# Kernel optimization log

Hardware: AMD Instinct MI355X
Metric: run time of the kernel (lower is better)

Reference implementation:

```python
import jax, jax.numpy as jnp
import numpy as np

B = 2; QD = 128; H = QD; W = QD; NQ = QD * QD
EMBED = 256; HEADS = 8; POINTS = 4; D = EMBED // HEADS; FFN = 512


def setup_inputs() -> dict:
    key = jax.random.key(0)
    ks = jax.random.split(key, 16)
    s = 0.02
    rn = lambda k, shp: jax.random.normal(k, shp, jnp.float32) * s
    return {
        'q': jax.random.normal(ks[0], (B, NQ, EMBED), jnp.float32),
        'W_off': rn(ks[1], (EMBED, HEADS * POINTS * 2)),
        'b_off': rn(ks[2], (HEADS * POINTS * 2,)),
        'W_attn': rn(ks[3], (EMBED, HEADS * POINTS)),
        'b_attn': rn(ks[4], (HEADS * POINTS,)),
        'W_val': rn(ks[5], (EMBED, EMBED)),
        'b_val': rn(ks[6], (EMBED,)),
        'W_out': rn(ks[7], (EMBED, EMBED)),
        'b_out': rn(ks[8], (EMBED,)),
        'W1': rn(ks[9], (EMBED, FFN)),
        'b1': rn(ks[10], (FFN,)),
        'W2': rn(ks[11], (FFN, EMBED)),
        'b2': rn(ks[12], (EMBED,)),
        'gamma': jnp.ones((EMBED,), jnp.float32),
        'beta': jnp.zeros((EMBED,), jnp.float32),
    }


def _layernorm(x, g, b):
    m = x.mean(-1, keepdims=True)
    v = ((x - m) ** 2).mean(-1, keepdims=True)
    return (x - m) * jax.lax.rsqrt(v + 1e-5) * g + b


def _msda(q, W_off, b_off, W_attn, b_attn, W_val, b_val, W_out, b_out):
    # value projection; value == query here. (B, NQ, EMBED)
    value = q @ W_val + b_val
    v = value.reshape(B, NQ, HEADS, D).transpose(0, 2, 1, 3)  # (B, heads, Nv, D)

    off = (q @ W_off + b_off).reshape(B, NQ, HEADS, POINTS, 2)
    aw = jax.nn.softmax((q @ W_attn + b_attn).reshape(B, NQ, HEADS, POINTS), axis=-1)

    # reference points: torch.meshgrid(linspace, linspace, indexing='xy')
    lin = jnp.linspace(0.0, 1.0, QD)
    gx, gy = jnp.meshgrid(lin, lin, indexing='xy')
    ref = jnp.stack([gx, gy], -1).reshape(1, NQ, 1, 1, 2)

    # offset_normalizer = [W, H]; sampling locations in [0,1]
    loc = ref + off / jnp.array([W, H], jnp.float32)
    # grid_sample bilinear, align_corners=False: pixel = loc * size - 0.5
    px = (loc[..., 0] * W - 0.5).transpose(0, 2, 1, 3)  # (B, heads, NQ, P)
    py = (loc[..., 1] * H - 0.5).transpose(0, 2, 1, 3)

    x0 = jnp.floor(px)
    y0 = jnp.floor(py)
    sampled = jnp.zeros((B, HEADS, NQ, POINTS, D), jnp.float32)
    for dy in (0.0, 1.0):
        for dx in (0.0, 1.0):
            xi = x0 + dx
            yi = y0 + dy
            wgt = (1.0 - jnp.abs(px - xi)) * (1.0 - jnp.abs(py - yi))
            valid = ((xi >= 0) & (xi <= W - 1) & (yi >= 0) & (yi <= H - 1)).astype(jnp.float32)
            idx = (jnp.clip(yi, 0, H - 1).astype(jnp.int32) * W
                   + jnp.clip(xi, 0, W - 1).astype(jnp.int32))  # (B, heads, NQ, P)
            g = jnp.take_along_axis(v, idx.reshape(B, HEADS, NQ * POINTS, 1), axis=2)
            g = g.reshape(B, HEADS, NQ, POINTS, D)
            sampled = sampled + g * (wgt * valid)[..., None]

    awt = aw.transpose(0, 2, 1, 3)  # (B, heads, NQ, P)
    out = (sampled * awt[..., None]).sum(3)  # (B, heads, NQ, D)
    out = out.transpose(0, 2, 1, 3).reshape(B, NQ, EMBED)
    # mmcv: dropout(output_proj(out)) + identity ; dropout is identity at eval
    return out @ W_out + b_out + q


def reference(q, W_off, b_off, W_attn, b_attn, W_val, b_val, W_out, b_out,
              W1, b1, W2, b2, gamma, beta):
    attn = _msda(q, W_off, b_off, W_attn, b_attn, W_val, b_val, W_out, b_out)
    x = attn + q  # outer residual in the module (in addition to mmcv's internal one)
    ffn = _layernorm(jax.nn.relu(x @ W1 + b1) @ W2 + b2, gamma, beta)
    return x + ffn
```

## Files before the change

### kernel.cpp

```cpp
#include <hip/hip_runtime.h>
#include <hip/hip_bf16.h>
#include <cstddef>
#include <cstdint>

#define B_      2
#define QD_     128
#define NQ_     (QD_ * QD_)
#define EMBED_  256
#define HEADS_  8
#define POINTS_ 4
#define FFN_    512
#define RTOT_   (B_ * NQ_)
#define NCATP_  384

using bf16x8 = __attribute__((ext_vector_type(8))) short;
using f32x4  = __attribute__((ext_vector_type(4))) float;

__device__ __forceinline__ short f2bf(float f) {
    unsigned u = __float_as_uint(f);
    u += 0x7FFFu + ((u >> 16) & 1u);
    return (short)(u >> 16);
}
__device__ __forceinline__ float bf2f(short s) {
    return __uint_as_float(((unsigned)(unsigned short)s) << 16);
}

#define GLDS(gp, lp) __builtin_amdgcn_global_load_lds( \
        (const __attribute__((address_space(1))) void*)(gp), \
        (__attribute__((address_space(3))) void*)(lp), 16, 0, 0)

#define WCAT_ELEMS  (NCATP_ * 256)
#define WOUT_ELEMS  (256 * 256)
#define W1_ELEMS    (512 * 256)
#define W2_ELEMS    (256 * 512)
#define PREP_TOTAL  (WCAT_ELEMS + WOUT_ELEMS + W1_ELEMS + W2_ELEMS)
#define PREP_BLOCKS ((PREP_TOTAL + 255) / 256)

__global__ __launch_bounds__(256) void prep_weights(
        const float* __restrict__ Wv, const float* __restrict__ Wo,
        const float* __restrict__ Wa, const float* __restrict__ bv,
        const float* __restrict__ bo, const float* __restrict__ ba,
        const float* __restrict__ W_out, const float* __restrict__ W1,
        const float* __restrict__ W2,
        short* __restrict__ WcatT, short* __restrict__ WoutT,
        short* __restrict__ W1T, short* __restrict__ W2T,
        float* __restrict__ bcat) {
    int idx = blockIdx.x * 256 + threadIdx.x;
    if (idx < WCAT_ELEMS) {
        int c = idx >> 8, k = idx & 255;
        float v = 0.f;
        if (c < 256)      v = Wv[k * 256 + c];
        else if (c < 320) v = Wo[k * 64 + (c - 256)];
        else if (c < 352) v = Wa[k * 32 + (c - 320)];
        WcatT[idx] = f2bf(v);
    } else if (idx < WCAT_ELEMS + WOUT_ELEMS) {
        int j = idx - WCAT_ELEMS; int c = j >> 8, k = j & 255;
        WoutT[j] = f2bf(W_out[k * 256 + c]);
    } else if (idx < WCAT_ELEMS + WOUT_ELEMS + W1_ELEMS) {
        int j = idx - (WCAT_ELEMS + WOUT_ELEMS); int c = j >> 8, k = j & 255;
        W1T[j] = f2bf(W1[k * 512 + c]);
    } else if (idx < PREP_TOTAL) {
        int j = idx - (WCAT_ELEMS + WOUT_ELEMS + W1_ELEMS); int c = j >> 9, k = j & 511;
        W2T[j] = f2bf(W2[k * 256 + c]);
    }
    if (idx < NCATP_) {
        float v = 0.f;
        if (idx < 256)      v = bv[idx];
        else if (idx < 320) v = bo[idx - 256];
        else if (idx < 352) v = ba[idx - 320];
        bcat[idx] = v;
    }
}

__global__ __launch_bounds__(512) void gemm1_fused(
        const float* __restrict__ q,
        const short* __restrict__ WcatT,
        const float* __restrict__ bcat,
        short* __restrict__ qbf,
        short* __restrict__ vcomp,
        float* __restrict__ pm) {
    __shared__ __align__(16) short xs[128 * 256];
    __shared__ __align__(16) short Bs[2][128 * 64];

    const int t    = threadIdx.x;
    const int ln   = t & 63;
    const int w    = t >> 6;
    const int wr   = w >> 2;
    const int wc   = w & 3;
    const int lrow = ln & 15;
    const int lkg  = ln >> 4;
    const int row0 = blockIdx.x * 128;
    const int orow = lkg * 4;
    const int ocol = lrow;

    auto stage_b = [&](int step, int buf) {
        const int p  = step >> 2;
        const int kt = step & 3;
        #pragma unroll
        for (int j = 0; j < 2; ++j) {
            const int c0 = (w * 2 + j) * 64;
            const int c  = c0 + ln;
            const int r  = c >> 3;
            const int s  = (c & 7) ^ (r & 7);
            GLDS(WcatT + (size_t)(p * 128 + r) * 256 + kt * 64 + s * 8,
                 &Bs[buf][c0 * 8]);
        }
    };

    stage_b(0, 0);
    #pragma unroll
    for (int j = 0; j < 8; ++j) {
        const int c = t + 512 * j;
        const int r = c >> 5;
        const int s = c & 31;
        const float* qp = q + (size_t)(row0 + r) * 256 + s * 8;
        const float4 f0 = *(const float4*)qp;
        const float4 f1 = *(const float4*)(qp + 4);
        bf16x8 v;
        v[0] = f2bf(f0.x); v[1] = f2bf(f0.y); v[2] = f2bf(f0.z); v[3] = f2bf(f0.w);
        v[4] = f2bf(f1.x); v[5] = f2bf(f1.y); v[6] = f2bf(f1.z); v[7] = f2bf(f1.w);
        *(bf16x8*)&qbf[(size_t)(row0 + r) * 256 + s * 8] = v;
        const int kt = s >> 3, sc = s & 7;
        *(bf16x8*)&xs[kt * 8192 + r * 64 + (sc ^ (r & 7)) * 8] = v;
    }
    __syncthreads();

    f32x4 acc[4][2] = {};
    const f32x4 zero = {0.f, 0.f, 0.f, 0.f};

    int buf = 0;
    #pragma unroll 1
    for (int step = 0; step < 12; ++step) {
        if (step < 11) stage_b(step + 1, buf ^ 1);
        const int kt = step & 3;
        #pragma unroll
        for (int ks = 0; ks < 2; ++ks) {
            const int slot = ((ks * 4 + lkg) ^ (lrow & 7)) * 8;
            bf16x8 af[4], bfr[2];
            #pragma unroll
            for (int m = 0; m < 4; ++m)
                af[m] = *(const bf16x8*)&xs[kt * 8192 + (wr * 64 + m * 16 + lrow) * 64 + slot];
            #pragma unroll
            for (int n = 0; n < 2; ++n)
                bfr[n] = *(const bf16x8*)&Bs[buf][(wc * 32 + n * 16 + lrow) * 64 + slot];
            #pragma unroll
            for (int m = 0; m < 4; ++m)
                #pragma unroll
                for (int n = 0; n < 2; ++n)
                    acc[m][n] = __builtin_amdgcn_mfma_f32_16x16x32_bf16(
                        af[m], bfr[n], acc[m][n], 0, 0, 0);
        }
        __syncthreads();
        if ((step & 3) == 3) {
            const int p = step >> 2;
            #pragma unroll
            for (int m = 0; m < 4; ++m) {
                #pragma unroll
                for (int n = 0; n < 2; ++n) {
                    const int gcol = p * 128 + wc * 32 + n * 16 + ocol;
                    const float bv = bcat[gcol];
                    #pragma unroll
                    for (int rr = 0; rr < 4; ++rr) {
                        const int row = wr * 64 + m * 16 + orow + rr;
                        const float v = acc[m][n][rr] + bv;
                        if (gcol < 256) {
                            vcomp[(size_t)(row0 + row) * 256 + gcol] = f2bf(v);
                        } else {
                            const int cc = gcol - 256;
                            if (cc < 96)
                                pm[(size_t)(row0 + row) * 128 + cc] = v;
                        }
                    }
                    acc[m][n] = zero;
                }
            }
        }
        buf ^= 1;
    }
}

__global__ __launch_bounds__(512) void gemm_x_ffn1(
        const short* __restrict__ msda,
        const short* __restrict__ WoutT,
        const float* __restrict__ b_out,
        const short* __restrict__ qbf,
        const short* __restrict__ W1T,
        const float* __restrict__ b1,
        short* __restrict__ xbf,
        short* __restrict__ hid) {
    __shared__ __align__(16) short xs[128 * 256];
    __shared__ __align__(16) short stg[128 * 192];
    short* As = stg;
    short* Bs = stg + 128 * 64;

    const int t    = threadIdx.x;
    const int ln   = t & 63;
    const int w    = t >> 6;
    const int wr   = w >> 2;
    const int wc   = w & 3;
    const int lrow = ln & 15;
    const int lkg  = ln >> 4;
    const int row0 = blockIdx.x * 128;
    const int orow = lkg * 4;
    const int ocol = lrow;

    f32x4 acc[4][4] = {};
    for (int kt = 0; kt < 4; ++kt) {
        #pragma unroll
        for (int j = 0; j < 2; ++j) {
            const int c0 = (w * 2 + j) * 64;
            const int cc = c0 + ln;
            const int r  = cc >> 3;
            const int s  = (cc & 7) ^ (r & 7);
            GLDS(msda + (size_t)(row0 + r) * 256 + kt * 64 + s * 8, &As[c0 * 8]);
        }
        #pragma unroll
        for (int j = 0; j < 4; ++j) {
            const int c0 = (w * 4 + j) * 64;
            const int cc = c0 + ln;
            const int r  = cc >> 3;
            const int s  = (cc & 7) ^ (r & 7);
            GLDS(WoutT + (size_t)r * 256 + kt * 64 + s * 8, &Bs[c0 * 8]);
        }
        __syncthreads();
        #pragma unroll
        for (int ks = 0; ks < 2; ++ks) {
            const int slot = ((ks * 4 + lkg) ^ (lrow & 7)) * 8;
            bf16x8 af[4], bfr[4];
            #pragma unroll
            for (int m = 0; m < 4; ++m)
                af[m] = *(const bf16x8*)&As[(wr * 64 + m * 16 + lrow) * 64 + slot];
            #pragma unroll
            for (int n = 0; n < 4; ++n)
                bfr[n] = *(const bf16x8*)&Bs[(wc * 64 + n * 16 + lrow) * 64 + slot];
            #pragma unroll
            for (int m = 0; m < 4; ++m)
                #pragma unroll
                for (int n = 0; n < 4; ++n)
                    acc[m][n] = __builtin_amdgcn_mfma_f32_16x16x32_bf16(
                        af[m], bfr[n], acc[m][n], 0, 0, 0);
        }
        __syncthreads();
    }

    #pragma unroll
    for (int m = 0; m < 4; ++m) {
        #pragma unroll
        for (int n = 0; n < 4; ++n) {
            const int kk  = n * 16 + ocol;
            const int col = wc * 64 + kk;
            const float bv = b_out[col];
            #pragma unroll
            for (int rr = 0; rr < 4; ++rr) {
                const int row = wr * 64 + m * 16 + orow + rr;
                float v = acc[m][n][rr] + bv
                        + 2.f * bf2f(qbf[(size_t)(row0 + row) * 256 + col]);
                const short bb = f2bf(v);
                xbf[(size_t)(row0 + row) * 256 + col] = bb;
                xs[wc * 8192 + row * 64 + ((kk >> 3) ^ (row & 7)) * 8 + (kk & 7)] = bb;
            }
        }
    }
    __syncthreads();

    #pragma unroll 1
    for (int p = 0; p < 2; ++p) {
        f32x4 acc2[4][4] = {};
        for (int kt = 0; kt < 4; ++kt) {
            #pragma unroll
            for (int j = 0; j < 4; ++j) {
                const int c0 = (w * 4 + j) * 64;
                const int cc = c0 + ln;
                const int r  = cc >> 3;
                const int s  = (cc & 7) ^ (r & 7);
                GLDS(W1T + (size_t)(p * 256 + r) * 256 + kt * 64 + s * 8, &Bs[c0 * 8]);
            }
            __syncthreads();
            #pragma unroll
            for (int ks = 0; ks < 2; ++ks) {
                const int slot = ((ks * 4 + lkg) ^ (lrow & 7)) * 8;
                bf16x8 af[4], bfr[4];
                #pragma unroll
                for (int m = 0; m < 4; ++m)
                    af[m] = *(const bf16x8*)&xs[kt * 8192 + (wr * 64 + m * 16 + lrow) * 64 + slot];
                #pragma unroll
                for (int n = 0; n < 4; ++n)
                    bfr[n] = *(const bf16x8*)&Bs[(wc * 64 + n * 16 + lrow) * 64 + slot];
                #pragma unroll
                for (int m = 0; m < 4; ++m)
                    #pragma unroll
                    for (int n = 0; n < 4; ++n)
                        acc2[m][n] = __builtin_amdgcn_mfma_f32_16x16x32_bf16(
                            af[m], bfr[n], acc2[m][n], 0, 0, 0);
            }
            __syncthreads();
        }
        #pragma unroll
        for (int m = 0; m < 4; ++m) {
            #pragma unroll
            for (int n = 0; n < 4; ++n) {
                const int col = p * 256 + wc * 64 + n * 16 + ocol;
                const float bv = b1[col];
                #pragma unroll
                for (int rr = 0; rr < 4; ++rr) {
                    const int row = wr * 64 + m * 16 + orow + rr;
                    hid[(size_t)(row0 + row) * 512 + col] =
                        f2bf(fmaxf(acc2[m][n][rr] + bv, 0.f));
                }
            }
        }
    }
}

__global__ __launch_bounds__(256) void gemm_ln(
        const short* __restrict__ A,
        const short* __restrict__ Bt,
        const float* __restrict__ bias,
        const short* __restrict__ xres,
        const float* __restrict__ gamma, const float* __restrict__ beta,
        float* __restrict__ out, int M, int K) {
    __shared__ __align__(16) short As[2][64 * 64];
    __shared__ __align__(16) short Bs[256 * 64];
    __shared__ float red[64][4][2];

    const int t    = threadIdx.x;
    const int ln   = t & 63;
    const int w    = t >> 6;
    const int lrow = ln & 15;
    const int lkg  = ln >> 4;
    const int row0 = blockIdx.x * 64;

    f32x4 acc[4][4] = {};

    auto stage_a = [&](int buf, int k0) {
        #pragma unroll
        for (int j = 0; j < 2; ++j) {
            const int c0 = (w * 2 + j) * 64;
            const int c  = c0 + ln;
            const int r  = c >> 3;
            const int s  = (c & 7) ^ (r & 7);
            GLDS(A + (size_t)(row0 + r) * K + (k0 + s * 8), &As[buf][c0 * 8]);
        }
    };
    auto stage_b = [&](int k0) {
        #pragma unroll
        for (int j = 0; j < 8; ++j) {
            const int c0 = (w * 8 + j) * 64;
            const int c  = c0 + ln;
            const int r  = c >> 3;
            const int s  = (c & 7) ^ (r & 7);
            GLDS(Bt + (size_t)r * K + (k0 + s * 8), &Bs[c0 * 8]);
        }
    };

    stage_a(0, 0);
    stage_b(0);
    __syncthreads();
    int buf = 0;
    for (int kt = 0; kt < 8; ++kt) {
        if (kt < 7) stage_a(buf ^ 1, kt * 64 + 64);
        #pragma unroll
        for (int ks = 0; ks < 2; ++ks) {
            const int slot = ((ks * 4 + lkg) ^ (lrow & 7)) * 8;
            bf16x8 af[4], bfr[4];
            #pragma unroll
            for (int m = 0; m < 4; ++m)
                af[m] = *(const bf16x8*)&As[buf][(m * 16 + lrow) * 64 + slot];
            #pragma unroll
            for (int n = 0; n < 4; ++n)
                bfr[n] = *(const bf16x8*)&Bs[(w * 64 + n * 16 + lrow) * 64 + slot];
            #pragma unroll
            for (int m = 0; m < 4; ++m)
                #pragma unroll
                for (int n = 0; n < 4; ++n)
                    acc[m][n] = __builtin_amdgcn_mfma_f32_16x16x32_bf16(
                        af[m], bfr[n], acc[m][n], 0, 0, 0);
        }
        __syncthreads();
        if (kt < 7) {
            stage_b(kt * 64 + 64);
            __syncthreads();
        }
        buf ^= 1;
    }

    const int orow = lkg * 4;
    const int ocol = lrow;

    #pragma unroll
    for (int n = 0; n < 4; ++n) {
        const float bv = bias[w * 64 + n * 16 + ocol];
        #pragma unroll
        for (int m = 0; m < 4; ++m)
            #pragma unroll
            for (int rr = 0; rr < 4; ++rr)
                acc[m][n][rr] += bv;
    }

    #pragma unroll
    for (int m = 0; m < 4; ++m) {
        #pragma unroll
        for (int rr = 0; rr < 4; ++rr) {
            float s = 0.f, sq = 0.f;
            #pragma unroll
            for (int n = 0; n < 4; ++n) {
                const float v = acc[m][n][rr];
                s += v; sq += v * v;
            }
            #pragma unroll
            for (int o = 1; o < 16; o <<= 1) {
                s  += __shfl_xor(s, o, 64);
                sq += __shfl_xor(sq, o, 64);
            }
            if (ocol == 0) {
                const int row = m * 16 + orow + rr;
                red[row][w][0] = s;
                red[row][w][1] = sq;
            }
        }
    }
    __syncthreads();

    #pragma unroll
    for (int m = 0; m < 4; ++m) {
        #pragma unroll
        for (int rr = 0; rr < 4; ++rr) {
            const int row = m * 16 + orow + rr;
            const float S  = red[row][0][0] + red[row][1][0] + red[row][2][0] + red[row][3][0];
            const float SQ = red[row][0][1] + red[row][1][1] + red[row][2][1] + red[row][3][1];
            const float mean = S * (1.0f / 256.0f);
            const float var  = SQ * (1.0f / 256.0f) - mean * mean;
            const float rs   = rsqrtf(var + 1e-5f);
            const size_t rbase = (size_t)(row0 + row) * 256;
            #pragma unroll
            for (int n = 0; n < 4; ++n) {
                const int col = w * 64 + n * 16 + ocol;
                out[rbase + col] = bf2f(xres[rbase + col])
                                 + (acc[m][n][rr] - mean) * rs * gamma[col] + beta[col];
            }
        }
    }
}

__global__ __launch_bounds__(256) void msda_sample(
        const float* __restrict__ pm, const short* __restrict__ vcomp,
        short* __restrict__ msda) {
    __shared__ int   s_off[8][32][4];
    __shared__ float s_c[8][32][4];

    const int t  = threadIdx.x;
    const int r0 = blockIdx.x * 8;
    const int bq = r0 >> 14;

    {
        const int g = t >> 5, cmb = t & 31, h = cmb >> 2, p = cmb & 3;
        const int r = r0 + g;
        const int n = r & (NQ_ - 1);
        const int gi = n >> 7, gj = n & 127;
        const float* pr = pm + (size_t)r * 128;

        const float l0 = pr[64 + h * 4 + 0], l1 = pr[64 + h * 4 + 1];
        const float l2 = pr[64 + h * 4 + 2], l3 = pr[64 + h * 4 + 3];
        const float mx = fmaxf(fmaxf(l0, l1), fmaxf(l2, l3));
        const float sum = expf(l0 - mx) + expf(l1 - mx) + expf(l2 - mx) + expf(l3 - mx);
        const float lp = pr[64 + h * 4 + p];
        const float aw = expf(lp - mx) / sum;

        const float ox = pr[h * 8 + p * 2 + 0];
        const float oy = pr[h * 8 + p * 2 + 1];
        const float px = (gj * (1.0f / 127.0f) + ox * (1.0f / 128.0f)) * 128.0f - 0.5f;
        const float py = (gi * (1.0f / 127.0f) + oy * (1.0f / 128.0f)) * 128.0f - 0.5f;
        const float x0f = floorf(px), y0f = floorf(py);
        const int   x0 = (int)x0f, y0 = (int)y0f;
        const float fx = px - x0f, fy = py - y0f;
        const int x0c = min(max(x0, 0), 127), x1c = min(max(x0 + 1, 0), 127);
        const int y0c = min(max(y0, 0), 127), y1c = min(max(y0 + 1, 0), 127);
        const float vx0 = ((unsigned)x0 <= 127u) ? 1.f : 0.f;
        const float vx1 = ((unsigned)(x0 + 1) <= 127u) ? 1.f : 0.f;
        const float vy0 = ((unsigned)y0 <= 127u) ? 1.f : 0.f;
        const float vy1 = ((unsigned)(y0 + 1) <= 127u) ? 1.f : 0.f;

        s_off[g][cmb][0] = (y0c * 128 + x0c) * 512;
        s_off[g][cmb][1] = (y0c * 128 + x1c) * 512;
        s_off[g][cmb][2] = (y1c * 128 + x0c) * 512;
        s_off[g][cmb][3] = (y1c * 128 + x1c) * 512;
        s_c[g][cmb][0] = aw * (1.f - fx) * (1.f - fy) * vx0 * vy0;
        s_c[g][cmb][1] = aw * fx * (1.f - fy) * vx1 * vy0;
        s_c[g][cmb][2] = aw * (1.f - fx) * fy * vx0 * vy1;
        s_c[g][cmb][3] = aw * fx * fy * vx1 * vy1;
    }
    __syncthreads();

    const int half = t >> 7;
    const int h    = (t >> 4) & 7;
    const int dd   = t & 15;
    const char* vb = (const char*)vcomp + ((size_t)bq * NQ_ * 256 + h * 32 + dd * 2) * 2;

    #pragma unroll
    for (int it = 0; it < 4; ++it) {
        const int g = it * 2 + half;
        float a0 = 0.f, a1 = 0.f;
        #pragma unroll
        for (int p = 0; p < 4; ++p) {
            const int cmb = h * 4 + p;
            #pragma unroll
            for (int k = 0; k < 4; ++k) {
                const unsigned u = *(const unsigned*)(vb + s_off[g][cmb][k]);
                const float c = s_c[g][cmb][k];
                a0 += c * __uint_as_float(u << 16);
                a1 += c * __uint_as_float(u & 0xffff0000u);
            }
        }
        const int r = r0 + g;
        const unsigned o = (unsigned)(unsigned short)f2bf(a0)
                         | ((unsigned)(unsigned short)f2bf(a1) << 16);
        *(unsigned*)&msda[(size_t)r * 256 + h * 32 + dd * 2] = o;
    }
}

extern "C" void kernel_launch(void* const* d_in, const int* in_sizes, int n_in,
                              void* d_out, int out_size, void* d_ws, size_t ws_size,
                              hipStream_t stream) {
    const float* q      = (const float*)d_in[0];
    const float* b_out  = (const float*)d_in[8];
    const float* b1     = (const float*)d_in[10];
    const float* b2     = (const float*)d_in[12];
    const float* gamma  = (const float*)d_in[13];
    const float* beta   = (const float*)d_in[14];

    float* out = (float*)d_out;

    char* w = (char*)d_ws;
    float* pm    = (float*)w; w += (size_t)RTOT_ * 128 * 4;
    short* vcomp = (short*)w; w += (size_t)RTOT_ * 256 * 2;
    short* qbf   = (short*)w; w += (size_t)RTOT_ * EMBED_ * 2;
    short* msda  = (short*)w; w += (size_t)RTOT_ * EMBED_ * 2;
    short* xbf   = (short*)w; w += (size_t)RTOT_ * EMBED_ * 2;
    short* hid   = (short*)w; w += (size_t)RTOT_ * FFN_ * 2;
    short* WcatT = (short*)w; w += WCAT_ELEMS * 2;
    short* WoutT = (short*)w; w += WOUT_ELEMS * 2;
    short* W1T   = (short*)w; w += W1_ELEMS * 2;
    short* W2T   = (short*)w; w += W2_ELEMS * 2;
    float* bcat  = (float*)w; w += NCATP_ * 4;

    prep_weights<<<PREP_BLOCKS, 256, 0, stream>>>(
        (const float*)d_in[5], (const float*)d_in[1], (const float*)d_in[3],
        (const float*)d_in[6], (const float*)d_in[2], (const float*)d_in[4],
        (const float*)d_in[7], (const float*)d_in[9], (const float*)d_in[11],
        WcatT, WoutT, W1T, W2T, bcat);

    gemm1_fused<<<RTOT_ / 128, 512, 0, stream>>>(
        q, WcatT, bcat, qbf, vcomp, pm);

    msda_sample<<<RTOT_ / 8, 256, 0, stream>>>(pm, vcomp, msda);

    gemm_x_ffn1<<<RTOT_ / 128, 512, 0, stream>>>(
        msda, WoutT, b_out, qbf, W1T, b1, xbf, hid);

    gemm_ln<<<RTOT_ / 64, 256, 0, stream>>>(
        hid, W2T, b2, xbf, gamma, beta, out, RTOT_, FFN_);
}
```

Before: 101.1 us.

## Fuse deformable sampling into output-projection/FFN1 kernel via shared-memory staging

```diff
diff --git a/kernel.cpp b/kernel.cpp
--- a/kernel.cpp
+++ b/kernel.cpp
@@ -179,8 +179,9 @@
     }
 }
 
-__global__ __launch_bounds__(512) void gemm_x_ffn1(
-        const short* __restrict__ msda,
+__global__ __launch_bounds__(512) void msda_x_ffn1(
+        const float* __restrict__ pm,
+        const short* __restrict__ vcomp,
         const short* __restrict__ WoutT,
         const float* __restrict__ b_out,
         const short* __restrict__ qbf,
@@ -188,10 +189,11 @@
         const float* __restrict__ b1,
         short* __restrict__ xbf,
         short* __restrict__ hid) {
-    __shared__ __align__(16) short xs[128 * 256];
+    __shared__ __align__(16) short ms[128 * 256];
     __shared__ __align__(16) short stg[128 * 192];
-    short* As = stg;
-    short* Bs = stg + 128 * 64;
+    int*   s_off = (int*)stg;
+    float* s_c   = (float*)(stg + 8192);
+    short* Bs    = stg;
 
     const int t    = threadIdx.x;
     const int ln   = t & 63;
@@ -201,19 +203,87 @@
     const int lrow = ln & 15;
     const int lkg  = ln >> 4;
     const int row0 = blockIdx.x * 128;
+    const int bq   = row0 >> 14;
     const int orow = lkg * 4;
     const int ocol = lrow;
 
+    const int gh  = (t >> 4) & 7;
+    const int gdd = t & 15;
+    const char* vb = (const char*)vcomp
+                   + ((size_t)bq * NQ_ * 256 + gh * 32 + gdd * 2) * 2;
+
+    #pragma unroll 1
+    for (int c4 = 0; c4 < 4; ++c4) {
+        const int rr0 = c4 * 32;
+        #pragma unroll
+        for (int j = 0; j < 2; ++j) {
+            const int u = t + 512 * j;
+            const int g = u >> 5, cmb = u & 31, h = cmb >> 2, p = cmb & 3;
+            const int r = row0 + rr0 + g;
+            const int n = r & (NQ_ - 1);
+            const int gi = n >> 7, gj = n & 127;
+            const float* pr = pm + (size_t)r * 128;
+
+            const float l0 = pr[64 + h * 4 + 0], l1 = pr[64 + h * 4 + 1];
+            const float l2 = pr[64 + h * 4 + 2], l3 = pr[64 + h * 4 + 3];
+            const float mx = fmaxf(fmaxf(l0, l1), fmaxf(l2, l3));
+            const float sum = expf(l0 - mx) + expf(l1 - mx) + expf(l2 - mx) + expf(l3 - mx);
+            const float aw = expf(pr[64 + h * 4 + p] - mx) / sum;
+
+            const float ox = pr[h * 8 + p * 2 + 0];
+            const float oy = pr[h * 8 + p * 2 + 1];
+            const float px = (gj * (1.0f / 127.0f) + ox * (1.0f / 128.0f)) * 128.0f - 0.5f;
+            const float py = (gi * (1.0f / 127.0f) + oy * (1.0f / 128.0f)) * 128.0f - 0.5f;
+            const float x0f = floorf(px), y0f = floorf(py);
+            const int   x0 = (int)x0f, y0 = (int)y0f;
+            const float fx = px - x0f, fy = py - y0f;
+            const int x0c = min(max(x0, 0), 127), x1c = min(max(x0 + 1, 0), 127);
+            const int y0c = min(max(y0, 0), 127), y1c = min(max(y0 + 1, 0), 127);
+            const float vx0 = ((unsigned)x0 <= 127u) ? 1.f : 0.f;
+            const float vx1 = ((unsigned)(x0 + 1) <= 127u) ? 1.f : 0.f;
+            const float vy0 = ((unsigned)y0 <= 127u) ? 1.f : 0.f;
+            const float vy1 = ((unsigned)(y0 + 1) <= 127u) ? 1.f : 0.f;
+
+            const int base = (g * 32 + cmb) * 4;
+            s_off[base + 0] = (y0c * 128 + x0c) * 512;
+            s_off[base + 1] = (y0c * 128 + x1c) * 512;
+            s_off[base + 2] = (y1c * 128 + x0c) * 512;
+            s_off[base + 3] = (y1c * 128 + x1c) * 512;
+            s_c[base + 0] = aw * (1.f - fx) * (1.f - fy) * vx0 * vy0;
+            s_c[base + 1] = aw * fx * (1.f - fy) * vx1 * vy0;
+            s_c[base + 2] = aw * (1.f - fx) * fy * vx0 * vy1;
+            s_c[base + 3] = aw * fx * fy * vx1 * vy1;
+        }
+        __syncthreads();
+        #pragma unroll
+        for (int j = 0; j < 8; ++j) {
+            const int g = (t >> 7) + 4 * j;
+            float a0 = 0.f, a1 = 0.f;
+            #pragma unroll
+            for (int p = 0; p < 4; ++p) {
+                const int base = (g * 32 + gh * 4 + p) * 4;
+                #pragma unroll
+                for (int k = 0; k < 4; ++k) {
+                    const unsigned u = *(const unsigned*)(vb + s_off[base + k]);
+                    const float c = s_c[base + k];
+                    a0 += c * __uint_as_float(u << 16);
+                    a1 += c * __uint_as_float(u & 0xffff0000u);
+                }
+            }
+            const int row = rr0 + g;
+            const int col = gh * 32 + gdd * 2;
+            const int sect = col >> 6, kk = col & 63;
+            const unsigned o = (unsigned)(unsigned short)f2bf(a0)
+                             | ((unsigned)(unsigned short)f2bf(a1) << 16);
+            *(unsigned*)&ms[sect * 8192 + row * 64
+                            + ((kk >> 3) ^ (row & 7)) * 8 + (kk & 7)] = o;
+        }
+        __syncthreads();
+    }
+
     f32x4 acc[4][4] = {};
+    #pragma unroll 1
     for (int kt = 0; kt < 4; ++kt) {
-        #pragma unroll
-        for (int j = 0; j < 2; ++j) {
-            const int c0 = (w * 2 + j) * 64;
-            const int cc = c0 + ln;
-            const int r  = cc >> 3;
-            const int s  = (cc & 7) ^ (r & 7);
-            GLDS(msda + (size_t)(row0 + r) * 256 + kt * 64 + s * 8, &As[c0 * 8]);
-        }
         #pragma unroll
         for (int j = 0; j < 4; ++j) {
             const int c0 = (w * 4 + j) * 64;
@@ -229,7 +299,7 @@
             bf16x8 af[4], bfr[4];
             #pragma unroll
             for (int m = 0; m < 4; ++m)
-                af[m] = *(const bf16x8*)&As[(wr * 64 + m * 16 + lrow) * 64 + slot];
+                af[m] = *(const bf16x8*)&ms[kt * 8192 + (wr * 64 + m * 16 + lrow) * 64 + slot];
             #pragma unroll
             for (int n = 0; n < 4; ++n)
                 bfr[n] = *(const bf16x8*)&Bs[(wc * 64 + n * 16 + lrow) * 64 + slot];
@@ -257,7 +327,7 @@
                         + 2.f * bf2f(qbf[(size_t)(row0 + row) * 256 + col]);
                 const short bb = f2bf(v);
                 xbf[(size_t)(row0 + row) * 256 + col] = bb;
-                xs[wc * 8192 + row * 64 + ((kk >> 3) ^ (row & 7)) * 8 + (kk & 7)] = bb;
+                ms[wc * 8192 + row * 64 + ((kk >> 3) ^ (row & 7)) * 8 + (kk & 7)] = bb;
             }
         }
     }
@@ -266,6 +336,7 @@
     #pragma unroll 1
     for (int p = 0; p < 2; ++p) {
         f32x4 acc2[4][4] = {};
+        #pragma unroll 1
         for (int kt = 0; kt < 4; ++kt) {
             #pragma unroll
             for (int j = 0; j < 4; ++j) {
@@ -282,7 +353,7 @@
                 bf16x8 af[4], bfr[4];
                 #pragma unroll
                 for (int m = 0; m < 4; ++m)
-                    af[m] = *(const bf16x8*)&xs[kt * 8192 + (wr * 64 + m * 16 + lrow) * 64 + slot];
+                    af[m] = *(const bf16x8*)&ms[kt * 8192 + (wr * 64 + m * 16 + lrow) * 64 + slot];
                 #pragma unroll
                 for (int n = 0; n < 4; ++n)
                     bfr[n] = *(const bf16x8*)&Bs[(wc * 64 + n * 16 + lrow) * 64 + slot];
@@ -442,82 +513,6 @@
     }
 }
 
-__global__ __launch_bounds__(256) void msda_sample(
-        const float* __restrict__ pm, const short* __restrict__ vcomp,
-        short* __restrict__ msda) {
-    __shared__ int   s_off[8][32][4];
-    __shared__ float s_c[8][32][4];
-
-    const int t  = threadIdx.x;
-    const int r0 = blockIdx.x * 8;
-    const int bq = r0 >> 14;
-
-    {
-        const int g = t >> 5, cmb = t & 31, h = cmb >> 2, p = cmb & 3;
-        const int r = r0 + g;
-        const int n = r & (NQ_ - 1);
-        const int gi = n >> 7, gj = n & 127;
-        const float* pr = pm + (size_t)r * 128;
-
-        const float l0 = pr[64 + h * 4 + 0], l1 = pr[64 + h * 4 + 1];
-        const float l2 = pr[64 + h * 4 + 2], l3 = pr[64 + h * 4 + 3];
-        const float mx = fmaxf(fmaxf(l0, l1), fmaxf(l2, l3));
-        const float sum = expf(l0 - mx) + expf(l1 - mx) + expf(l2 - mx) + expf(l3 - mx);
-        const float lp = pr[64 + h * 4 + p];
-        const float aw = expf(lp - mx) / sum;
-
-        const float ox = pr[h * 8 + p * 2 + 0];
-        const float oy = pr[h * 8 + p * 2 + 1];
-        const float px = (gj * (1.0f / 127.0f) + ox * (1.0f / 128.0f)) * 128.0f - 0.5f;
-        const float py = (gi * (1.0f / 127.0f) + oy * (1.0f / 128.0f)) * 128.0f - 0.5f;
-        const float x0f = floorf(px), y0f = floorf(py);
-        const int   x0 = (int)x0f, y0 = (int)y0f;
-        const float fx = px - x0f, fy = py - y0f;
-        const int x0c = min(max(x0, 0), 127), x1c = min(max(x0 + 1, 0), 127);
-        const int y0c = min(max(y0, 0), 127), y1c = min(max(y0 + 1, 0), 127);
-        const float vx0 = ((unsigned)x0 <= 127u) ? 1.f : 0.f;
-        const float vx1 = ((unsigned)(x0 + 1) <= 127u) ? 1.f : 0.f;
-        const float vy0 = ((unsigned)y0 <= 127u) ? 1.f : 0.f;
-        const float vy1 = ((unsigned)(y0 + 1) <= 127u) ? 1.f : 0.f;
-
-        s_off[g][cmb][0] = (y0c * 128 + x0c) * 512;
-        s_off[g][cmb][1] = (y0c * 128 + x1c) * 512;
-        s_off[g][cmb][2] = (y1c * 128 + x0c) * 512;
-        s_off[g][cmb][3] = (y1c * 128 + x1c) * 512;
-        s_c[g][cmb][0] = aw * (1.f - fx) * (1.f - fy) * vx0 * vy0;
-        s_c[g][cmb][1] = aw * fx * (1.f - fy) * vx1 * vy0;
-        s_c[g][cmb][2] = aw * (1.f - fx) * fy * vx0 * vy1;
-        s_c[g][cmb][3] = aw * fx * fy * vx1 * vy1;
-    }
-    __syncthreads();
-
-    const int half = t >> 7;
-    const int h    = (t >> 4) & 7;
-    const int dd   = t & 15;
-    const char* vb = (const char*)vcomp + ((size_t)bq * NQ_ * 256 + h * 32 + dd * 2) * 2;
-
-    #pragma unroll
-    for (int it = 0; it < 4; ++it) {
-        const int g = it * 2 + half;
-        float a0 = 0.f, a1 = 0.f;
-        #pragma unroll
-        for (int p = 0; p < 4; ++p) {
-            const int cmb = h * 4 + p;
-            #pragma unroll
-            for (int k = 0; k < 4; ++k) {
-                const unsigned u = *(const unsigned*)(vb + s_off[g][cmb][k]);
-                const float c = s_c[g][cmb][k];
-                a0 += c * __uint_as_float(u << 16);
-                a1 += c * __uint_as_float(u & 0xffff0000u);
-            }
-        }
-        const int r = r0 + g;
-        const unsigned o = (unsigned)(unsigned short)f2bf(a0)
-                         | ((unsigned)(unsigned short)f2bf(a1) << 16);
-        *(unsigned*)&msda[(size_t)r * 256 + h * 32 + dd * 2] = o;
-    }
-}
-
 extern "C" void kernel_launch(void* const* d_in, const int* in_sizes, int n_in,
                               void* d_out, int out_size, void* d_ws, size_t ws_size,
                               hipStream_t stream) {
@@ -534,7 +529,6 @@
     float* pm    = (float*)w; w += (size_t)RTOT_ * 128 * 4;
     short* vcomp = (short*)w; w += (size_t)RTOT_ * 256 * 2;
     short* qbf   = (short*)w; w += (size_t)RTOT_ * EMBED_ * 2;
-    short* msda  = (short*)w; w += (size_t)RTOT_ * EMBED_ * 2;
     short* xbf   = (short*)w; w += (size_t)RTOT_ * EMBED_ * 2;
     short* hid   = (short*)w; w += (size_t)RTOT_ * FFN_ * 2;
     short* WcatT = (short*)w; w += WCAT_ELEMS * 2;
@@ -552,10 +546,8 @@
     gemm1_fused<<<RTOT_ / 128, 512, 0, stream>>>(
         q, WcatT, bcat, qbf, vcomp, pm);
 
-    msda_sample<<<RTOT_ / 8, 256, 0, stream>>>(pm, vcomp, msda);
-
-    gemm_x_ffn1<<<RTOT_ / 128, 512, 0, stream>>>(
-        msda, WoutT, b_out, qbf, W1T, b1, xbf, hid);
+    msda_x_ffn1<<<RTOT_ / 128, 512, 0, stream>>>(
+        pm, vcomp, WoutT, b_out, qbf, W1T, b1, xbf, hid);
 
     gemm_ln<<<RTOT_ / 64, 256, 0, stream>>>(
         hid, W2T, b2, xbf, gamma, beta, out, RTOT_, FFN_);
```

Result: slower. 117.9 us (+16.6%).

## Shrink GEMM row tiles to 64 rows with 256-thread blocks and restage pipelining

Applied to the files above, without the earlier changes.

```diff
diff --git a/kernel.cpp b/kernel.cpp
--- a/kernel.cpp
+++ b/kernel.cpp
@@ -72,24 +72,22 @@
     }
 }
 
-__global__ __launch_bounds__(512) void gemm1_fused(
+__global__ __launch_bounds__(256) void gemm1_fused(
         const float* __restrict__ q,
         const short* __restrict__ WcatT,
         const float* __restrict__ bcat,
         short* __restrict__ qbf,
         short* __restrict__ vcomp,
         float* __restrict__ pm) {
-    __shared__ __align__(16) short xs[128 * 256];
+    __shared__ __align__(16) short xs[64 * 256];
     __shared__ __align__(16) short Bs[2][128 * 64];
 
     const int t    = threadIdx.x;
     const int ln   = t & 63;
     const int w    = t >> 6;
-    const int wr   = w >> 2;
-    const int wc   = w & 3;
     const int lrow = ln & 15;
     const int lkg  = ln >> 4;
-    const int row0 = blockIdx.x * 128;
+    const int row0 = blockIdx.x * 64;
     const int orow = lkg * 4;
     const int ocol = lrow;
 
@@ -97,8 +95,8 @@
         const int p  = step >> 2;
         const int kt = step & 3;
         #pragma unroll
-        for (int j = 0; j < 2; ++j) {
-            const int c0 = (w * 2 + j) * 64;
+        for (int j = 0; j < 4; ++j) {
+            const int c0 = (w * 4 + j) * 64;
             const int c  = c0 + ln;
             const int r  = c >> 3;
             const int s  = (c & 7) ^ (r & 7);
@@ -110,7 +108,7 @@
     stage_b(0, 0);
     #pragma unroll
     for (int j = 0; j < 8; ++j) {
-        const int c = t + 512 * j;
+        const int c = t + 256 * j;
         const int r = c >> 5;
         const int s = c & 31;
         const float* qp = q + (size_t)(row0 + r) * 256 + s * 8;
@@ -121,7 +119,7 @@
         v[4] = f2bf(f1.x); v[5] = f2bf(f1.y); v[6] = f2bf(f1.z); v[7] = f2bf(f1.w);
         *(bf16x8*)&qbf[(size_t)(row0 + r) * 256 + s * 8] = v;
         const int kt = s >> 3, sc = s & 7;
-        *(bf16x8*)&xs[kt * 8192 + r * 64 + (sc ^ (r & 7)) * 8] = v;
+        *(bf16x8*)&xs[kt * 4096 + r * 64 + (sc ^ (r & 7)) * 8] = v;
     }
     __syncthreads();
 
@@ -139,10 +137,10 @@
             bf16x8 af[4], bfr[2];
             #pragma unroll
             for (int m = 0; m < 4; ++m)
-                af[m] = *(const bf16x8*)&xs[kt * 8192 + (wr * 64 + m * 16 + lrow) * 64 + slot];
+                af[m] = *(const bf16x8*)&xs[kt * 4096 + (m * 16 + lrow) * 64 + slot];
             #pragma unroll
             for (int n = 0; n < 2; ++n)
-                bfr[n] = *(const bf16x8*)&Bs[buf][(wc * 32 + n * 16 + lrow) * 64 + slot];
+                bfr[n] = *(const bf16x8*)&Bs[buf][(w * 32 + n * 16 + lrow) * 64 + slot];
             #pragma unroll
             for (int m = 0; m < 4; ++m)
                 #pragma unroll
@@ -157,11 +155,11 @@
             for (int m = 0; m < 4; ++m) {
                 #pragma unroll
                 for (int n = 0; n < 2; ++n) {
-                    const int gcol = p * 128 + wc * 32 + n * 16 + ocol;
+                    const int gcol = p * 128 + w * 32 + n * 16 + ocol;
                     const float bv = bcat[gcol];
                     #pragma unroll
                     for (int rr = 0; rr < 4; ++rr) {
-                        const int row = wr * 64 + m * 16 + orow + rr;
+                        const int row = m * 16 + orow + rr;
                         const float v = acc[m][n][rr] + bv;
                         if (gcol < 256) {
                             vcomp[(size_t)(row0 + row) * 256 + gcol] = f2bf(v);
@@ -176,269 +174,6 @@
             }
         }
         buf ^= 1;
-    }
-}
-
-__global__ __launch_bounds__(512) void gemm_x_ffn1(
-        const short* __restrict__ msda,
-        const short* __restrict__ WoutT,
-        const float* __restrict__ b_out,
-        const short* __restrict__ qbf,
-        const short* __restrict__ W1T,
-        const float* __restrict__ b1,
-        short* __restrict__ xbf,
-        short* __restrict__ hid) {
-    __shared__ __align__(16) short xs[128 * 256];
-    __shared__ __align__(16) short stg[128 * 192];
-    short* As = stg;
-    short* Bs = stg + 128 * 64;
-
-    const int t    = threadIdx.x;
-    const int ln   = t & 63;
-    const int w    = t >> 6;
-    const int wr   = w >> 2;
-    const int wc   = w & 3;
-    const int lrow = ln & 15;
-    const int lkg  = ln >> 4;
-    const int row0 = blockIdx.x * 128;
-    const int orow = lkg * 4;
-    const int ocol = lrow;
-
-    f32x4 acc[4][4] = {};
-    for (int kt = 0; kt < 4; ++kt) {
-        #pragma unroll
-        for (int j = 0; j < 2; ++j) {
-            const int c0 = (w * 2 + j) * 64;
-            const int cc = c0 + ln;
-            const int r  = cc >> 3;
-            const int s  = (cc & 7) ^ (r & 7);
-            GLDS(msda + (size_t)(row0 + r) * 256 + kt * 64 + s * 8, &As[c0 * 8]);
-        }
-        #pragma unroll
-        for (int j = 0; j < 4; ++j) {
-            const int c0 = (w * 4 + j) * 64;
-            const int cc = c0 + ln;
-            const int r  = cc >> 3;
-            const int s  = (cc & 7) ^ (r & 7);
-            GLDS(WoutT + (size_t)r * 256 + kt * 64 + s * 8, &Bs[c0 * 8]);
-        }
-        __syncthreads();
-        #pragma unroll
-        for (int ks = 0; ks < 2; ++ks) {
-            const int slot = ((ks * 4 + lkg) ^ (lrow & 7)) * 8;
-            bf16x8 af[4], bfr[4];
-            #pragma unroll
-            for (int m = 0; m < 4; ++m)
-                af[m] = *(const bf16x8*)&As[(wr * 64 + m * 16 + lrow) * 64 + slot];
-            #pragma unroll
-            for (int n = 0; n < 4; ++n)
-                bfr[n] = *(const bf16x8*)&Bs[(wc * 64 + n * 16 + lrow) * 64 + slot];
-            #pragma unroll
-            for (int m = 0; m < 4; ++m)
-                #pragma unroll
-                for (int n = 0; n < 4; ++n)
-                    acc[m][n] = __builtin_amdgcn_mfma_f32_16x16x32_bf16(
-                        af[m], bfr[n], acc[m][n], 0, 0, 0);
-        }
-        __syncthreads();
-    }
-
-    #pragma unroll
-    for (int m = 0; m < 4; ++m) {
-        #pragma unroll
-        for (int n = 0; n < 4; ++n) {
-            const int kk  = n * 16 + ocol;
-            const int col = wc * 64 + kk;
-            const float bv = b_out[col];
-            #pragma unroll
-            for (int rr = 0; rr < 4; ++rr) {
-                const int row = wr * 64 + m * 16 + orow + rr;
-                float v = acc[m][n][rr] + bv
-                        + 2.f * bf2f(qbf[(size_t)(row0 + row) * 256 + col]);
-                const short bb = f2bf(v);
-                xbf[(size_t)(row0 + row) * 256 + col] = bb;
-                xs[wc * 8192 + row * 64 + ((kk >> 3) ^ (row & 7)) * 8 + (kk & 7)] = bb;
-            }
-        }
-    }
-    __syncthreads();
-
-    #pragma unroll 1
-    for (int p = 0; p < 2; ++p) {
-        f32x4 acc2[4][4] = {};
-        for (int kt = 0; kt < 4; ++kt) {
-            #pragma unroll
-            for (int j = 0; j < 4; ++j) {
-                const int c0 = (w * 4 + j) * 64;
-                const int cc = c0 + ln;
-                const int r  = cc >> 3;
-                const int s  = (cc & 7) ^ (r & 7);
-                GLDS(W1T + (size_t)(p * 256 + r) * 256 + kt * 64 + s * 8, &Bs[c0 * 8]);
-            }
-            __syncthreads();
-            #pragma unroll
-            for (int ks = 0; ks < 2; ++ks) {
-                const int slot = ((ks * 4 + lkg) ^ (lrow & 7)) * 8;
-                bf16x8 af[4], bfr[4];
-                #pragma unroll
-                for (int m = 0; m < 4; ++m)
-                    af[m] = *(const bf16x8*)&xs[kt * 8192 + (wr * 64 + m * 16 + lrow) * 64 + slot];
-                #pragma unroll
-                for (int n = 0; n < 4; ++n)
-                    bfr[n] = *(const bf16x8*)&Bs[(wc * 64 + n * 16 + lrow) * 64 + slot];
-                #pragma unroll
-                for (int m = 0; m < 4; ++m)
-                    #pragma unroll
-                    for (int n = 0; n < 4; ++n)
-                        acc2[m][n] = __builtin_amdgcn_mfma_f32_16x16x32_bf16(
-                            af[m], bfr[n], acc2[m][n], 0, 0, 0);
-            }
-            __syncthreads();
-        }
-        #pragma unroll
-        for (int m = 0; m < 4; ++m) {
-            #pragma unroll
-            for (int n = 0; n < 4; ++n) {
-                const int col = p * 256 + wc * 64 + n * 16 + ocol;
-                const float bv = b1[col];
-                #pragma unroll
-                for (int rr = 0; rr < 4; ++rr) {
-                    const int row = wr * 64 + m * 16 + orow + rr;
-                    hid[(size_t)(row0 + row) * 512 + col] =
-                        f2bf(fmaxf(acc2[m][n][rr] + bv, 0.f));
-                }
-            }
-        }
-    }
-}
-
-__global__ __launch_bounds__(256) void gemm_ln(
-        const short* __restrict__ A,
-        const short* __restrict__ Bt,
-        const float* __restrict__ bias,
-        const short* __restrict__ xres,
-        const float* __restrict__ gamma, const float* __restrict__ beta,
-        float* __restrict__ out, int M, int K) {
-    __shared__ __align__(16) short As[2][64 * 64];
-    __shared__ __align__(16) short Bs[256 * 64];
-    __shared__ float red[64][4][2];
-
-    const int t    = threadIdx.x;
-    const int ln   = t & 63;
-    const int w    = t >> 6;
-    const int lrow = ln & 15;
-    const int lkg  = ln >> 4;
-    const int row0 = blockIdx.x * 64;
-
-    f32x4 acc[4][4] = {};
-
-    auto stage_a = [&](int buf, int k0) {
-        #pragma unroll
-        for (int j = 0; j < 2; ++j) {
-            const int c0 = (w * 2 + j) * 64;
-            const int c  = c0 + ln;
-            const int r  = c >> 3;
-            const int s  = (c & 7) ^ (r & 7);
-            GLDS(A + (size_t)(row0 + r) * K + (k0 + s * 8), &As[buf][c0 * 8]);
-        }
-    };
-    auto stage_b = [&](int k0) {
-        #pragma unroll
-        for (int j = 0; j < 8; ++j) {
-            const int c0 = (w * 8 + j) * 64;
-            const int c  = c0 + ln;
-            const int r  = c >> 3;
-            const int s  = (c & 7) ^ (r & 7);
-            GLDS(Bt + (size_t)r * K + (k0 + s * 8), &Bs[c0 * 8]);
-        }
-    };
-
-    stage_a(0, 0);
-    stage_b(0);
-    __syncthreads();
-    int buf = 0;
-    for (int kt = 0; kt < 8; ++kt) {
-        if (kt < 7) stage_a(buf ^ 1, kt * 64 + 64);
-        #pragma unroll
-        for (int ks = 0; ks < 2; ++ks) {
-            const int slot = ((ks * 4 + lkg) ^ (lrow & 7)) * 8;
-            bf16x8 af[4], bfr[4];
-            #pragma unroll
-            for (int m = 0; m < 4; ++m)
-                af[m] = *(const bf16x8*)&As[buf][(m * 16 + lrow) * 64 + slot];
-            #pragma unroll
-            for (int n = 0; n < 4; ++n)
-                bfr[n] = *(const bf16x8*)&Bs[(w * 64 + n * 16 + lrow) * 64 + slot];
-            #pragma unroll
-            for (int m = 0; m < 4; ++m)
-                #pragma unroll
-                for (int n = 0; n < 4; ++n)
-                    acc[m][n] = __builtin_amdgcn_mfma_f32_16x16x32_bf16(
-                        af[m], bfr[n], acc[m][n], 0, 0, 0);
-        }
-        __syncthreads();
-        if (kt < 7) {
-            stage_b(kt * 64 + 64);
-            __syncthreads();
-        }
-        buf ^= 1;
-    }
-
-    const int orow = lkg * 4;
-    const int ocol = lrow;
-
-    #pragma unroll
-    for (int n = 0; n < 4; ++n) {
-        const float bv = bias[w * 64 + n * 16 + ocol];
-        #pragma unroll
-        for (int m = 0; m < 4; ++m)
-            #pragma unroll
-            for (int rr = 0; rr < 4; ++rr)
-                acc[m][n][rr] += bv;
-    }
-
-    #pragma unroll
-    for (int m = 0; m < 4; ++m) {
-        #pragma unroll
-        for (int rr = 0; rr < 4; ++rr) {
-            float s = 0.f, sq = 0.f;
-            #pragma unroll
-            for (int n = 0; n < 4; ++n) {
-                const float v = acc[m][n][rr];
-                s += v; sq += v * v;
-            }
-            #pragma unroll
-            for (int o = 1; o < 16; o <<= 1) {
-                s  += __shfl_xor(s, o, 64);
-                sq += __shfl_xor(sq, o, 64);
-            }
-            if (ocol == 0) {
-                const int row = m * 16 + orow + rr;
-                red[row][w][0] = s;
-                red[row][w][1] = sq;
-            }
-        }
-    }
-    __syncthreads();
-
-    #pragma unroll
-    for (int m = 0; m < 4; ++m) {
-        #pragma unroll
-        for (int rr = 0; rr < 4; ++rr) {
-            const int row = m * 16 + orow + rr;
-            const float S  = red[row][0][0] + red[row][1][0] + red[row][2][0] + red[row][3][0];
-            const float SQ = red[row][0][1] + red[row][1][1] + red[row][2][1] + red[row][3][1];
-            const float mean = S * (1.0f / 256.0f);
-            const float var  = SQ * (1.0f / 256.0f) - mean * mean;
-            const float rs   = rsqrtf(var + 1e-5f);
-            const size_t rbase = (size_t)(row0 + row) * 256;
-            #pragma unroll
-            for (int n = 0; n < 4; ++n) {
-                const int col = w * 64 + n * 16 + ocol;
-                out[rbase + col] = bf2f(xres[rbase + col])
-                                 + (acc[m][n][rr] - mean) * rs * gamma[col] + beta[col];
-            }
-        }
     }
 }
 
@@ -518,6 +253,285 @@
     }
 }
 
+__global__ __launch_bounds__(256) void gemm_x_ffn1(
+        const short* __restrict__ msda,
+        const short* __restrict__ WoutT,
+        const float* __restrict__ b_out,
+        const short* __restrict__ qbf,
+        const short* __restrict__ W1T,
+        const float* __restrict__ b1,
+        short* __restrict__ xbf,
+        short* __restrict__ hid) {
+    __shared__ __align__(16) short xs[64 * 256];
+    __shared__ __align__(16) short As[2][64 * 64];
+    __shared__ __align__(16) short Bs[256 * 64];
+
+    const int t    = threadIdx.x;
+    const int ln   = t & 63;
+    const int w    = t >> 6;
+    const int lrow = ln & 15;
+    const int lkg  = ln >> 4;
+    const int row0 = blockIdx.x * 64;
+    const int orow = lkg * 4;
+    const int ocol = lrow;
+
+    auto stage_a = [&](int buf, int kt) {
+        #pragma unroll
+        for (int j = 0; j < 2; ++j) {
+            const int c0 = (w * 2 + j) * 64;
+            const int c  = c0 + ln;
+            const int r  = c >> 3;
+            const int s  = (c & 7) ^ (r & 7);
+            GLDS(msda + (size_t)(row0 + r) * 256 + kt * 64 + s * 8, &As[buf][c0 * 8]);
+        }
+    };
+    auto stage_b1 = [&](int kt) {
+        #pragma unroll
+        for (int j = 0; j < 8; ++j) {
+            const int c0 = (w * 8 + j) * 64;
+            const int c  = c0 + ln;
+            const int r  = c >> 3;
+            const int s  = (c & 7) ^ (r & 7);
+            GLDS(WoutT + (size_t)r * 256 + kt * 64 + s * 8, &Bs[c0 * 8]);
+        }
+    };
+    auto stage_b2 = [&](int p, int kt) {
+        #pragma unroll
+        for (int j = 0; j < 8; ++j) {
+            const int c0 = (w * 8 + j) * 64;
+            const int c  = c0 + ln;
+            const int r  = c >> 3;
+            const int s  = (c & 7) ^ (r & 7);
+            GLDS(W1T + (size_t)(p * 256 + r) * 256 + kt * 64 + s * 8, &Bs[c0 * 8]);
+        }
+    };
+
+    f32x4 acc[4][4] = {};
+    stage_a(0, 0);
+    stage_b1(0);
+    __syncthreads();
+    int buf = 0;
+    #pragma unroll 1
+    for (int kt = 0; kt < 4; ++kt) {
+        if (kt < 3) stage_a(buf ^ 1, kt + 1);
+        #pragma unroll
+        for (int ks = 0; ks < 2; ++ks) {
+            const int slot = ((ks * 4 + lkg) ^ (lrow & 7)) * 8;
+            bf16x8 af[4], bfr[4];
+            #pragma unroll
+            for (int m = 0; m < 4; ++m)
+                af[m] = *(const bf16x8*)&As[buf][(m * 16 + lrow) * 64 + slot];
+            #pragma unroll
+            for (int n = 0; n < 4; ++n)
+                bfr[n] = *(const bf16x8*)&Bs[(w * 64 + n * 16 + lrow) * 64 + slot];
+            #pragma unroll
+            for (int m = 0; m < 4; ++m)
+                #pragma unroll
+                for (int n = 0; n < 4; ++n)
+                    acc[m][n] = __builtin_amdgcn_mfma_f32_16x16x32_bf16(
+                        af[m], bfr[n], acc[m][n], 0, 0, 0);
+        }
+        __syncthreads();
+        if (kt < 3) {
+            stage_b1(kt + 1);
+            __syncthreads();
+        }
+        buf ^= 1;
+    }
+
+    #pragma unroll
+    for (int m = 0; m < 4; ++m) {
+        #pragma unroll
+        for (int n = 0; n < 4; ++n) {
+            const int kk  = n * 16 + ocol;
+            const int col = w * 64 + kk;
+            const float bv = b_out[col];
+            #pragma unroll
+            for (int rr = 0; rr < 4; ++rr) {
+                const int row = m * 16 + orow + rr;
+                float v = acc[m][n][rr] + bv
+                        + 2.f * bf2f(qbf[(size_t)(row0 + row) * 256 + col]);
+                const short bb = f2bf(v);
+                xbf[(size_t)(row0 + row) * 256 + col] = bb;
+                xs[w * 4096 + row * 64 + ((kk >> 3) ^ (row & 7)) * 8 + (kk & 7)] = bb;
+            }
+        }
+    }
+    __syncthreads();
+
+    #pragma unroll 1
+    for (int p = 0; p < 2; ++p) {
+        f32x4 acc2[4][4] = {};
+        #pragma unroll 1
+        for (int kt = 0; kt < 4; ++kt) {
+            stage_b2(p, kt);
+            __syncthreads();
+            #pragma unroll
+            for (int ks = 0; ks < 2; ++ks) {
+                const int slot = ((ks * 4 + lkg) ^ (lrow & 7)) * 8;
+                bf16x8 af[4], bfr[4];
+                #pragma unroll
+                for (int m = 0; m < 4; ++m)
+                    af[m] = *(const bf16x8*)&xs[kt * 4096 + (m * 16 + lrow) * 64 + slot];
+                #pragma unroll
+                for (int n = 0; n < 4; ++n)
+                    bfr[n] = *(const bf16x8*)&Bs[(w * 64 + n * 16 + lrow) * 64 + slot];
+                #pragma unroll
+                for (int m = 0; m < 4; ++m)
+                    #pragma unroll
+                    for (int n = 0; n < 4; ++n)
+                        acc2[m][n] = __builtin_amdgcn_mfma_f32_16x16x32_bf16(
+                            af[m], bfr[n], acc2[m][n], 0, 0, 0);
+            }
+            __syncthreads();
+        }
+        #pragma unroll
+        for (int m = 0; m < 4; ++m) {
+            #pragma unroll
+            for (int n = 0; n < 4; ++n) {
+                const int col = p * 256 + w * 64 + n * 16 + ocol;
+                const float bv = b1[col];
+                #pragma unroll
+                for (int rr = 0; rr < 4; ++rr) {
+                    const int row = m * 16 + orow + rr;
+                    hid[(size_t)(row0 + row) * 512 + col] =
+                        f2bf(fmaxf(acc2[m][n][rr] + bv, 0.f));
+                }
+            }
+        }
+    }
+}
+
+__global__ __launch_bounds__(256) void gemm_ln(
+        const short* __restrict__ A,
+        const short* __restrict__ Bt,
+        const float* __restrict__ bias,
+        const short* __restrict__ xres,
+        const float* __restrict__ gamma, const float* __restrict__ beta,
+        float* __restrict__ out, int M, int K) {
+    __shared__ __align__(16) short As[2][64 * 64];
+    __shared__ __align__(16) short Bs[256 * 64];
+    __shared__ float red[64][4][2];
+
+    const int t    = threadIdx.x;
+    const int ln   = t & 63;
+    const int w    = t >> 6;
+    const int lrow = ln & 15;
+    const int lkg  = ln >> 4;
+    const int row0 = blockIdx.x * 64;
+
+    f32x4 acc[4][4] = {};
+
+    auto stage_a = [&](int buf, int k0) {
+        #pragma unroll
+        for (int j = 0; j < 2; ++j) {
+            const int c0 = (w * 2 + j) * 64;
+            const int c  = c0 + ln;
+            const int r  = c >> 3;
+            const int s  = (c & 7) ^ (r & 7);
+            GLDS(A + (size_t)(row0 + r) * K + (k0 + s * 8), &As[buf][c0 * 8]);
+        }
+    };
+    auto stage_b = [&](int k0) {
+        #pragma unroll
+        for (int j = 0; j < 8; ++j) {
+            const int c0 = (w * 8 + j) * 64;
+            const int c  = c0 + ln;
+            const int r  = c >> 3;
+            const int s  = (c & 7) ^ (r & 7);
+            GLDS(Bt + (size_t)r * K + (k0 + s * 8), &Bs[c0 * 8]);
+        }
+    };
+
+    stage_a(0, 0);
+    stage_b(0);
+    __syncthreads();
+    int buf = 0;
+    for (int kt = 0; kt < 8; ++kt) {
+        if (kt < 7) stage_a(buf ^ 1, kt * 64 + 64);
+        #pragma unroll
+        for (int ks = 0; ks < 2; ++ks) {
+            const int slot = ((ks * 4 + lkg) ^ (lrow & 7)) * 8;
+            bf16x8 af[4], bfr[4];
+            #pragma unroll
+            for (int m = 0; m < 4; ++m)
+                af[m] = *(const bf16x8*)&As[buf][(m * 16 + lrow) * 64 + slot];
+            #pragma unroll
+            for (int n = 0; n < 4; ++n)
+                bfr[n] = *(const bf16x8*)&Bs[(w * 64 + n * 16 + lrow) * 64 + slot];
+            #pragma unroll
+            for (int m = 0; m < 4; ++m)
+                #pragma unroll
+                for (int n = 0; n < 4; ++n)
+                    acc[m][n] = __builtin_amdgcn_mfma_f32_16x16x32_bf16(
+                        af[m], bfr[n], acc[m][n], 0, 0, 0);
+        }
+        __syncthreads();
+        if (kt < 7) {
+            stage_b(kt * 64 + 64);
+            __syncthreads();
+        }
+        buf ^= 1;
+    }
+
+    const int orow = lkg * 4;
+    const int ocol = lrow;
+
+    #pragma unroll
+    for (int n = 0; n < 4; ++n) {
+        const float bv = bias[w * 64 + n * 16 + ocol];
+        #pragma unroll
+        for (int m = 0; m < 4; ++m)
+            #pragma unroll
+            for (int rr = 0; rr < 4; ++rr)
+                acc[m][n][rr] += bv;
+    }
+
+    #pragma unroll
+    for (int m = 0; m < 4; ++m) {
+        #pragma unroll
+        for (int rr = 0; rr < 4; ++rr) {
+            float s = 0.f, sq = 0.f;
+            #pragma unroll
+            for (int n = 0; n < 4; ++n) {
+                const float v = acc[m][n][rr];
+                s += v; sq += v * v;
+            }
+            #pragma unroll
+            for (int o = 1; o < 16; o <<= 1) {
+                s  += __shfl_xor(s, o, 64);
+                sq += __shfl_xor(sq, o, 64);
+            }
+            if (ocol == 0) {
+                const int row = m * 16 + orow + rr;
+                red[row][w][0] = s;
+                red[row][w][1] = sq;
+            }
+        }
+    }
+    __syncthreads();
+
+    #pragma unroll
+    for (int m = 0; m < 4; ++m) {
+        #pragma unroll
+        for (int rr = 0; rr < 4; ++rr) {
+            const int row = m * 16 + orow + rr;
+            const float S  = red[row][0][0] + red[row][1][0] + red[row][2][0] + red[row][3][0];
+            const float SQ = red[row][0][1] + red[row][1][1] + red[row][2][1] + red[row][3][1];
+            const float mean = S * (1.0f / 256.0f);
+            const float var  = SQ * (1.0f / 256.0f) - mean * mean;
+            const float rs   = rsqrtf(var + 1e-5f);
+            const size_t rbase = (size_t)(row0 + row) * 256;
+            #pragma unroll
+            for (int n = 0; n < 4; ++n) {
+                const int col = w * 64 + n * 16 + ocol;
+                out[rbase + col] = bf2f(xres[rbase + col])
+                                 + (acc[m][n][rr] - mean) * rs * gamma[col] + beta[col];
+            }
+        }
+    }
+}
+
 extern "C" void kernel_launch(void* const* d_in, const int* in_sizes, int n_in,
                               void* d_out, int out_size, void* d_ws, size_t ws_size,
                               hipStream_t stream) {
@@ -549,12 +563,12 @@
         (const float*)d_in[7], (const float*)d_in[9], (const float*)d_in[11],
         WcatT, WoutT, W1T, W2T, bcat);
 
-    gemm1_fused<<<RTOT_ / 128, 512, 0, stream>>>(
+    gemm1_fused<<<RTOT_ / 64, 256, 0, stream>>>(
         q, WcatT, bcat, qbf, vcomp, pm);
 
     msda_sample<<<RTOT_ / 8, 256, 0, stream>>>(pm, vcomp, msda);
 
-    gemm_x_ffn1<<<RTOT_ / 128, 512, 0, stream>>>(
+    gemm_x_ffn1<<<RTOT_ / 64, 256, 0, stream>>>(
         msda, WoutT, b_out, qbf, W1T, b1, xbf, hid);
 
     gemm_ln<<<RTOT_ / 64, 256, 0, stream>>>(
```

Result: slower. 116.6 us (+15.3%).
